# Kernel optimization log

Hardware: AMD Instinct MI355X
Metric: run time of the kernel (lower is better)

The kernel has to match this reference:

```python
import jax, jax.numpy as jnp
import numpy as np
from jax import lax

NEG = -9.0e15
ALPHA = 0.2  # LeakyReLU slope

def _cnn(x, conv1_w, conv1_b, conv2_w, conv2_b):
    # x: (BN,1,9,9)
    dn = ('NCHW', 'OIHW', 'NCHW')
    y = lax.conv_general_dilated(x, conv1_w, (1, 1), 'SAME', dimension_numbers=dn)
    y = jax.nn.relu(y + conv1_b[None, :, None, None])
    y = lax.conv_general_dilated(y, conv2_w, (1, 1), 'VALID', dimension_numbers=dn)
    y = jax.nn.relu(y + conv2_b[None, :, None, None])
    return y.reshape(y.shape[0], -1)  # (BN, 32*7*7=1568)

def _gat(h, adj, W, a1, a2):
    # h: (B,N,F) ; adj: (B,N,N) int
    Wh = h @ W                                  # (B,N,D)
    # a([Wh_i ; Wh_j]) == Wh_i@a1 + Wh_j@a2  (exact split of the concat linear)
    s1 = Wh @ a1                                # (B,N) query-node term
    s2 = Wh @ a2                                # (B,N) key-node term
    e = jax.nn.leaky_relu(s1[:, :, None] + s2[:, None, :], ALPHA)  # (B,N,N)
    e = jnp.where(adj > 0, e, NEG)
    attn = jax.nn.softmax(e, axis=-1)           # dropout off (eval mode)
    h_prime = jnp.einsum('bij,bjd->bid', attn, Wh)
    return jax.nn.elu(h_prime)

def reference(obs_grids, adj_matrix, conv1_w, conv1_b, conv2_w, conv2_b,
              W, a1, a2, actor_w, actor_b, critic_w, critic_b):
    B, N, C, H, Wd = obs_grids.shape
    feats = _cnn(obs_grids.reshape(B * N, C, H, Wd), conv1_w, conv1_b, conv2_w, conv2_b)
    feats = feats.reshape(B, N, -1)             # (B,N,1568)
    emb = _gat(feats, adj_matrix, W, a1, a2)    # (B,N,64)
    logits = emb @ actor_w + actor_b            # (B,N,n_actions)
    values = emb @ critic_w + critic_b          # (B,N,1)
    return (logits, values)

def setup_inputs() -> dict:
    key = jax.random.key(0)
    ks = jax.random.split(key, 12)
    B, N, H, Wd = 8, 1024, 9, 9
    FEAT, HID, NA = 1568, 64, 16
    f32 = jnp.float32
    inp = {}
    inp['obs_grids'] = jax.random.normal(ks[0], (B, N, 1, H, Wd), f32)
    inp['adj_matrix'] = jax.random.randint(ks[1], (B, N, N), 0, 2, jnp.int32)
    inp['conv1_w'] = jax.random.normal(ks[2], (16, 1, 3, 3), f32) * 0.1
    inp['conv1_b'] = jnp.zeros((16,), f32)
    inp['conv2_w'] = jax.random.normal(ks[3], (32, 16, 3, 3), f32) * 0.05
    inp['conv2_b'] = jnp.zeros((32,), f32)
    inp['W'] = jax.random.normal(ks[4], (FEAT, HID), f32) * (1.0 / np.sqrt(FEAT))
    inp['a1'] = jax.random.normal(ks[5], (HID,), f32) * 0.1
    inp['a2'] = jax.random.normal(ks[6], (HID,), f32) * 0.1
    inp['actor_w'] = jax.random.normal(ks[7], (HID, NA), f32) * (1.0 / np.sqrt(HID))
    inp['actor_b'] = jnp.zeros((NA,), f32)
    inp['critic_w'] = jax.random.normal(ks[8], (HID, 1), f32) * (1.0 / np.sqrt(HID))
    inp['critic_b'] = jnp.zeros((1,), f32)
    return inp
```

## Files before the change

kernel.cpp:

```cpp
#include <hip/hip_runtime.h>
#include <math.h>

#define NEG_BIG (-9.0e15f)

typedef __attribute__((ext_vector_type(8))) short short8;
typedef __attribute__((ext_vector_type(4))) short short4v;
typedef __attribute__((ext_vector_type(4))) float f32x4;

__device__ __forceinline__ short f32_to_bf16_bits(float f) {
  union { float f; unsigned u; } cv; cv.f = f;
  unsigned r = (cv.u + 0x7fffu + ((cv.u >> 16) & 1u)) >> 16;
  return (short)r;
}

__global__ __launch_bounds__(256) void wt_prep(const float* __restrict__ W,
                                               short* __restrict__ Wt) {
  int idx = blockIdx.x * 256 + threadIdx.x;
  if (idx < 1568 * 64) {
    int k = idx >> 6, n = idx & 63;
    Wt[n * 1568 + k] = f32_to_bf16_bits(W[idx]);
  }
}

#define IPB 8
#define FSTR 1608
__global__ __launch_bounds__(256) void cnn_gemm_kernel(
    const float* __restrict__ obs, const float* __restrict__ w1,
    const float* __restrict__ b1, const float* __restrict__ w2,
    const float* __restrict__ b2, const short* __restrict__ Wt,
    const float* __restrict__ a1, const float* __restrict__ a2,
    short* __restrict__ Whb, float* __restrict__ s1, float* __restrict__ s2)
{
  __shared__ float sw1[144];
  __shared__ float sb1[16];
  __shared__ float sb2[32];
  __shared__ __align__(16) short wt[32 * 160];
  __shared__ float sinp[IPB * 121];
  __shared__ __align__(16) short ubuf[IPB * FSTR];
  int tid = threadIdx.x;
  long inst0 = (long)blockIdx.x * IPB;

  for (int i = tid; i < 144; i += 256) sw1[i] = w1[i];
  if (tid < 16) sb1[tid] = b1[tid];
  if (tid < 32) sb2[tid] = b2[tid];
  for (int i = tid; i < 32 * 160; i += 256) {
    int o = i / 160, kp = i - o * 160;
    int kstep = kp >> 5, which = (kp >> 4) & 1, ci = kp & 15;
    int tap = kstep * 2 + which;
    float v = (tap < 9) ? w2[o * 144 + ci * 9 + tap] : 0.0f;
    wt[i] = f32_to_bf16_bits(v);
  }
  for (int i = tid; i < IPB * 121; i += 256) {
    int inst = i / 121, rem = i - inst * 121;
    int py = rem / 11, px = rem - py * 11;
    float v = 0.f;
    if (py >= 1 && py <= 9 && px >= 1 && px <= 9)
      v = obs[(inst0 + inst) * 81 + (py - 1) * 9 + (px - 1)];
    sinp[inst * 121 + rem] = v;
  }
  __syncthreads();

  {
    int inst = tid >> 5, s = tid & 31;
    const float* ib = &sinp[inst * 121];
    short* hw = &ubuf[inst * FSTR];
    for (int c = 0; c < 16; ++c) {
      float wk[9];
      #pragma unroll
      for (int k = 0; k < 9; ++k) wk[k] = sw1[c * 9 + k];
      float bias = sb1[c];
      #pragma unroll
      for (int t = 0; t < 3; ++t) {
        int px = s + t * 32;
        if (px < 81) {
          int y = (px * 456) >> 12;
          const float* ip = ib + px + 2 * y;
          float a = bias
            + ip[0]  * wk[0] + ip[1]  * wk[1] + ip[2]  * wk[2]
            + ip[11] * wk[3] + ip[12] * wk[4] + ip[13] * wk[5]
            + ip[22] * wk[6] + ip[23] * wk[7] + ip[24] * wk[8];
          a = fmaxf(a, 0.f);
          int idx = (px * 16 + c) ^ (((px >> 2) & 3) << 3);
          hw[idx] = f32_to_bf16_bits(a);
        }
      }
    }
  }

  int lane = tid & 63;
  int wv = tid >> 6;
  int g = lane >> 4;
  int which = g >> 1;
  int half = g & 1;
  int colr = lane & 15;

  const int offtab[9] = {0, 1, 2, 9, 10, 11, 18, 19, 20};
  int myoff[5];
  #pragma unroll
  for (int k = 0; k < 5; ++k) {
    int tap = k * 2 + which;
    myoff[k] = (tap < 9) ? offtab[tap] : 0;
  }
  int posm[4];
  #pragma unroll
  for (int mt = 0; mt < 4; ++mt) {
    int p = mt * 16 + colr;
    posm[mt] = (p < 49) ? (p / 7) * 9 + (p % 7) : 0;
  }
  short8 bfw[2][5];
  #pragma unroll
  for (int nt = 0; nt < 2; ++nt)
    #pragma unroll
    for (int k = 0; k < 5; ++k)
      bfw[nt][k] = *(const short8*)&wt[(nt * 16 + colr) * 160 + k * 32 + g * 8];

  #pragma unroll
  for (int ii = 0; ii < 2; ++ii) {
    int inst = wv * 2 + ii;
    const short* hb = &ubuf[inst * FSTR];
    short* fb = &ubuf[inst * FSTR];
    f32x4 acc[4][2];
    #pragma unroll
    for (int mt = 0; mt < 4; ++mt) {
      short8 af[5];
      #pragma unroll
      for (int k = 0; k < 5; ++k) {
        int row = posm[mt] + myoff[k];
        int idx = (row * 16 + half * 8) ^ (((row >> 2) & 3) << 3);
        af[k] = *(const short8*)&hb[idx];
      }
      #pragma unroll
      for (int nt = 0; nt < 2; ++nt) {
        f32x4 a0 = {0.f, 0.f, 0.f, 0.f};
        #pragma unroll
        for (int k = 0; k < 5; ++k)
          a0 = __builtin_amdgcn_mfma_f32_16x16x32_bf16(af[k], bfw[nt][k], a0, 0, 0, 0);
        acc[mt][nt] = a0;
      }
    }
    #pragma unroll
    for (int mt = 0; mt < 4; ++mt) {
      #pragma unroll
      for (int nt = 0; nt < 2; ++nt) {
        int o = nt * 16 + colr;
        float bias = sb2[o];
        #pragma unroll
        for (int r = 0; r < 4; ++r) {
          int p = mt * 16 + g * 4 + r;
          if (p < 49)
            fb[o * 49 + p] = f32_to_bf16_bits(fmaxf(acc[mt][nt][r] + bias, 0.f));
        }
      }
    }
  }
  __syncthreads();

  {
    int arow = colr & 7;
    const short* Wrow = Wt + (wv * 16 + colr) * 1568;
    f32x4 acc2 = {0.f, 0.f, 0.f, 0.f};
    for (int ks = 0; ks < 49; ++ks) {
      short8 af = *(const short8*)&ubuf[arow * FSTR + ks * 32 + g * 8];
      short8 bf = *(const short8*)&Wrow[ks * 32 + g * 8];
      acc2 = __builtin_amdgcn_mfma_f32_16x16x32_bf16(af, bf, acc2, 0, 0, 0);
    }
    float a1c = a1[wv * 16 + colr];
    float a2c = a2[wv * 16 + colr];
    float* sp1 = sinp;
    float* sp2 = sinp + 32;
    if (g < 2) {
      long bidx = inst0 >> 10;
      int node0 = (int)(inst0 & 1023) + g * 4;
      short4v pk;
      #pragma unroll
      for (int r = 0; r < 4; ++r) pk[r] = f32_to_bf16_bits(acc2[r]);
      *(short4v*)&Whb[(bidx * 64 + wv * 16 + colr) * 1024 + node0] = pk;
      #pragma unroll
      for (int r = 0; r < 4; ++r) {
        int inst = g * 4 + r;
        float v = acc2[r];
        float x1 = v * a1c, x2 = v * a2c;
        #pragma unroll
        for (int w = 1; w < 16; w <<= 1) { x1 += __shfl_xor(x1, w); x2 += __shfl_xor(x2, w); }
        if (colr == 0) { sp1[wv * 8 + inst] = x1; sp2[wv * 8 + inst] = x2; }
      }
    }
  }
  __syncthreads();
  if (tid < 8) {
    float* sp1 = sinp;
    float* sp2 = sinp + 32;
    s1[inst0 + tid] = sp1[tid] + sp1[8 + tid] + sp1[16 + tid] + sp1[24 + tid];
    s2[inst0 + tid] = sp2[tid] + sp2[8 + tid] + sp2[16 + tid] + sp2[24 + tid];
  }
}

#define PSTR2 1096
__global__ __launch_bounds__(256) void gat_kernel(
    const int* __restrict__ adj, const short* __restrict__ Whb,
    const float* __restrict__ s1, const float* __restrict__ s2,
    const float* __restrict__ actor_w, const float* __restrict__ actor_b,
    const float* __restrict__ critic_w, const float* __restrict__ critic_b,
    float* __restrict__ out)
{
  __shared__ __align__(16) short pb[16 * PSTR2];
  __shared__ __align__(16) float s2s[1024];
  __shared__ float saw[64 * 16];
  __shared__ float scw[64];
  __shared__ float sab[16];
  __shared__ float denom[16];
  __shared__ float emb[16][65];
  int tid = threadIdx.x;
  int b = blockIdx.y;
  int i0 = blockIdx.x * 16;

  for (int j = tid; j < 1024; j += 256) s2s[j] = s2[b * 1024 + j];
  for (int idx2 = tid; idx2 < 64 * 16; idx2 += 256) saw[idx2] = actor_w[idx2];
  if (tid < 64) scw[tid] = critic_w[tid];
  if (tid < 16) sab[tid] = actor_b[tid];
  __syncthreads();

  {
    int il = tid >> 4, r = tid & 15;
    int i = i0 + il;
    float s1i = s1[b * 1024 + i];
    const int* arow = adj + ((long)(b * 1024 + i)) * 1024;
    unsigned long long amask = 0ull;
    float m = -3.0e38f;
    #pragma unroll
    for (int jj = 0; jj < 16; ++jj) {
      int j0 = jj * 64 + r * 4;
      int4 a4 = *(const int4*)&arow[j0];
      float4 sv = *(const float4*)&s2s[j0];
      float e0 = s1i + sv.x; e0 = (e0 > 0.f) ? e0 : 0.2f * e0;
      float e1 = s1i + sv.y; e1 = (e1 > 0.f) ? e1 : 0.2f * e1;
      float e2 = s1i + sv.z; e2 = (e2 > 0.f) ? e2 : 0.2f * e2;
      float e3 = s1i + sv.w; e3 = (e3 > 0.f) ? e3 : 0.2f * e3;
      if (a4.x > 0) { m = fmaxf(m, e0); amask |= 1ull << (jj * 4 + 0); }
      if (a4.y > 0) { m = fmaxf(m, e1); amask |= 1ull << (jj * 4 + 1); }
      if (a4.z > 0) { m = fmaxf(m, e2); amask |= 1ull << (jj * 4 + 2); }
      if (a4.w > 0) { m = fmaxf(m, e3); amask |= 1ull << (jj * 4 + 3); }
    }
    #pragma unroll
    for (int w = 1; w < 16; w <<= 1) m = fmaxf(m, __shfl_xor(m, w));
    float sum = 0.f;
    short* prow = &pb[il * PSTR2];
    #pragma unroll
    for (int jj = 0; jj < 16; ++jj) {
      int j0 = jj * 64 + r * 4;
      float4 sv = *(const float4*)&s2s[j0];
      float e0 = s1i + sv.x; e0 = (e0 > 0.f) ? e0 : 0.2f * e0;
      float e1 = s1i + sv.y; e1 = (e1 > 0.f) ? e1 : 0.2f * e1;
      float e2 = s1i + sv.z; e2 = (e2 > 0.f) ? e2 : 0.2f * e2;
      float e3 = s1i + sv.w; e3 = (e3 > 0.f) ? e3 : 0.2f * e3;
      float p0 = ((amask >> (jj * 4 + 0)) & 1ull) ? __expf(e0 - m) : 0.f;
      float p1 = ((amask >> (jj * 4 + 1)) & 1ull) ? __expf(e1 - m) : 0.f;
      float p2 = ((amask >> (jj * 4 + 2)) & 1ull) ? __expf(e2 - m) : 0.f;
      float p3 = ((amask >> (jj * 4 + 3)) & 1ull) ? __expf(e3 - m) : 0.f;
      sum += (p0 + p1) + (p2 + p3);
      short4v st;
      st[0] = f32_to_bf16_bits(p0); st[1] = f32_to_bf16_bits(p1);
      st[2] = f32_to_bf16_bits(p2); st[3] = f32_to_bf16_bits(p3);
      *(short4v*)&prow[j0] = st;
    }
    #pragma unroll
    for (int w = 1; w < 16; w <<= 1) sum += __shfl_xor(sum, w);
    if (r == 0) denom[il] = sum;
  }
  __syncthreads();

  {
    int lane = tid & 63, wv = tid >> 6, g = lane >> 4, colr = lane & 15;
    const short* Wcol = Whb + ((long)b * 64 + wv * 16 + colr) * 1024;
    const short* prow = &pb[colr * PSTR2];
    f32x4 acc = {0.f, 0.f, 0.f, 0.f};
    #pragma unroll
    for (int ks = 0; ks < 32; ++ks) {
      short8 af = *(const short8*)&prow[ks * 32 + g * 8];
      short8 bf = *(const short8*)&Wcol[ks * 32 + g * 8];
      acc = __builtin_amdgcn_mfma_f32_16x16x32_bf16(af, bf, acc, 0, 0, 0);
    }
    #pragma unroll
    for (int rr = 0; rr < 4; ++rr) {
      int row = g * 4 + rr;
      float v = acc[rr] / denom[row];
      v = (v > 0.f) ? v : expm1f(v);
      emb[row][wv * 16 + colr] = v;
    }
  }
  __syncthreads();

  {
    int il = tid >> 4, na = tid & 15;
    float accl = sab[na];
    #pragma unroll
    for (int d = 0; d < 64; ++d) accl += emb[il][d] * saw[d * 16 + na];
    out[((long)(b * 1024 + i0 + il)) * 16 + na] = accl;
  }
  if (tid < 16) {
    float v = critic_b[0];
    #pragma unroll
    for (int d = 0; d < 64; ++d) v += emb[tid][d] * scw[d];
    out[131072 + b * 1024 + i0 + tid] = v;
  }
}

extern "C" void kernel_launch(void* const* d_in, const int* in_sizes, int n_in,
                              void* d_out, int out_size, void* d_ws, size_t ws_size,
                              hipStream_t stream)
{
  const float* obs = (const float*)d_in[0];
  const int*   adj = (const int*)d_in[1];
  const float* c1w = (const float*)d_in[2];
  const float* c1b = (const float*)d_in[3];
  const float* c2w = (const float*)d_in[4];
  const float* c2b = (const float*)d_in[5];
  const float* W   = (const float*)d_in[6];
  const float* a1  = (const float*)d_in[7];
  const float* a2  = (const float*)d_in[8];
  const float* aw  = (const float*)d_in[9];
  const float* ab  = (const float*)d_in[10];
  const float* cw  = (const float*)d_in[11];
  const float* cb  = (const float*)d_in[12];
  float* out = (float*)d_out;
  float* ws = (float*)d_ws;

  short* Whb = (short*)ws;
  float* s1  = ws + 262144;
  float* s2  = s1 + 8192;
  short* Wt  = (short*)(s2 + 8192);

  hipLaunchKernelGGL(wt_prep, dim3((1568 * 64 + 255) / 256), dim3(256), 0, stream, W, Wt);
  hipLaunchKernelGGL(cnn_gemm_kernel, dim3(1024), dim3(256), 0, stream,
                     obs, c1w, c1b, c2w, c2b, Wt, a1, a2, Whb, s1, s2);
  hipLaunchKernelGGL(gat_kernel, dim3(64, 8), dim3(256), 0, stream,
                     adj, Whb, s1, s2, aw, ab, cw, cb, out);
}
```

Baseline: 67.69 us.

## Pad CNN feature layout to 52 per channel and vectorize conv stores

Repacks the projection weight and the per-instance feature buffer so each of the 32 channels occupies 52 bf16 slots (49 valid plus zero padding). This allows conv2 outputs to be written as packed 4-element stores instead of guarded scalar stores. Conv1 now caches its input patch in registers, loads weights and bias as float4 vectors from a padded LDS table, and writes two channels per 32-bit store. The trade-off is that the projection GEMM runs 52 MFMA k-steps instead of 49, and the padded region must be zeroed in shared memory, which also grows LDS use.

```diff
diff --git a/kernel.cpp b/kernel.cpp
--- a/kernel.cpp
+++ b/kernel.cpp
@@ -13,17 +13,20 @@
   return (short)r;
 }
 
+#define KPAD 1664
 __global__ __launch_bounds__(256) void wt_prep(const float* __restrict__ W,
                                                short* __restrict__ Wt) {
   int idx = blockIdx.x * 256 + threadIdx.x;
-  if (idx < 1568 * 64) {
-    int k = idx >> 6, n = idx & 63;
-    Wt[n * 1568 + k] = f32_to_bf16_bits(W[idx]);
+  if (idx < 64 * KPAD) {
+    int n = idx / KPAD, kk = idx - n * KPAD;
+    int o = kk / 52, p = kk - o * 52;
+    float v = (p < 49) ? W[(o * 49 + p) * 64 + n] : 0.0f;
+    Wt[idx] = f32_to_bf16_bits(v);
   }
 }
 
 #define IPB 8
-#define FSTR 1608
+#define FSTR 1672
 __global__ __launch_bounds__(256) void cnn_gemm_kernel(
     const float* __restrict__ obs, const float* __restrict__ w1,
     const float* __restrict__ b1, const float* __restrict__ w2,
@@ -31,8 +34,7 @@
     const float* __restrict__ a1, const float* __restrict__ a2,
     short* __restrict__ Whb, float* __restrict__ s1, float* __restrict__ s2)
 {
-  __shared__ float sw1[144];
-  __shared__ float sb1[16];
+  __shared__ __align__(16) float sw1p[192];
   __shared__ float sb2[32];
   __shared__ __align__(16) short wt[32 * 160];
   __shared__ float sinp[IPB * 121];
@@ -40,8 +42,11 @@
   int tid = threadIdx.x;
   long inst0 = (long)blockIdx.x * IPB;
 
-  for (int i = tid; i < 144; i += 256) sw1[i] = w1[i];
-  if (tid < 16) sb1[tid] = b1[tid];
+  for (int i = tid; i < 192; i += 256) {
+    int c = i / 12, k = i - c * 12;
+    float v = (k < 9) ? w1[c * 9 + k] : ((k == 9) ? b1[c] : 0.0f);
+    sw1p[i] = v;
+  }
   if (tid < 32) sb2[tid] = b2[tid];
   for (int i = tid; i < 32 * 160; i += 256) {
     int o = i / 160, kp = i - o * 160;
@@ -58,30 +63,54 @@
       v = obs[(inst0 + inst) * 81 + (py - 1) * 9 + (px - 1)];
     sinp[inst * 121 + rem] = v;
   }
+  for (int i = tid; i < IPB * 188; i += 256) {
+    int inst = i / 188, q = i - inst * 188;
+    *(unsigned*)&ubuf[inst * FSTR + 1296 + q * 2] = 0u;
+  }
   __syncthreads();
 
   {
     int inst = tid >> 5, s = tid & 31;
     const float* ib = &sinp[inst * 121];
     short* hw = &ubuf[inst * FSTR];
-    for (int c = 0; c < 16; ++c) {
-      float wk[9];
-      #pragma unroll
-      for (int k = 0; k < 9; ++k) wk[k] = sw1[c * 9 + k];
-      float bias = sb1[c];
+    float inr[3][9];
+    #pragma unroll
+    for (int t = 0; t < 3; ++t) {
+      int px = s + t * 32;
+      if (px < 81) {
+        int y = (px * 456) >> 12;
+        const float* ip = ib + px + 2 * y;
+        inr[t][0] = ip[0];  inr[t][1] = ip[1];  inr[t][2] = ip[2];
+        inr[t][3] = ip[11]; inr[t][4] = ip[12]; inr[t][5] = ip[13];
+        inr[t][6] = ip[22]; inr[t][7] = ip[23]; inr[t][8] = ip[24];
+      }
+    }
+    #pragma unroll
+    for (int cp = 0; cp < 8; ++cp) {
+      int c0 = cp * 2, c1 = cp * 2 + 1;
+      float4 wa0 = *(const float4*)&sw1p[c0 * 12];
+      float4 wb0 = *(const float4*)&sw1p[c0 * 12 + 4];
+      float4 wc0 = *(const float4*)&sw1p[c0 * 12 + 8];
+      float4 wa1 = *(const float4*)&sw1p[c1 * 12];
+      float4 wb1 = *(const float4*)&sw1p[c1 * 12 + 4];
+      float4 wc1 = *(const float4*)&sw1p[c1 * 12 + 8];
       #pragma unroll
       for (int t = 0; t < 3; ++t) {
         int px = s + t * 32;
         if (px < 81) {
-          int y = (px * 456) >> 12;
-          const float* ip = ib + px + 2 * y;
-          float a = bias
-            + ip[0]  * wk[0] + ip[1]  * wk[1] + ip[2]  * wk[2]
-            + ip[11] * wk[3] + ip[12] * wk[4] + ip[13] * wk[5]
-            + ip[22] * wk[6] + ip[23] * wk[7] + ip[24] * wk[8];
-          a = fmaxf(a, 0.f);
-          int idx = (px * 16 + c) ^ (((px >> 2) & 3) << 3);
-          hw[idx] = f32_to_bf16_bits(a);
+          float v0 = wc0.y
+            + inr[t][0] * wa0.x + inr[t][1] * wa0.y + inr[t][2] * wa0.z
+            + inr[t][3] * wa0.w + inr[t][4] * wb0.x + inr[t][5] * wb0.y
+            + inr[t][6] * wb0.z + inr[t][7] * wb0.w + inr[t][8] * wc0.x;
+          float v1 = wc1.y
+            + inr[t][0] * wa1.x + inr[t][1] * wa1.y + inr[t][2] * wa1.z
+            + inr[t][3] * wa1.w + inr[t][4] * wb1.x + inr[t][5] * wb1.y
+            + inr[t][6] * wb1.z + inr[t][7] * wb1.w + inr[t][8] * wc1.x;
+          v0 = fmaxf(v0, 0.f); v1 = fmaxf(v1, 0.f);
+          unsigned pk = (unsigned)(unsigned short)f32_to_bf16_bits(v0)
+                      | ((unsigned)(unsigned short)f32_to_bf16_bits(v1) << 16);
+          int idx = (px * 16 + c0) ^ (((px >> 2) & 3) << 3);
+          *(unsigned*)&hw[idx] = pk;
         }
       }
     }
@@ -139,17 +168,23 @@
       }
     }
     #pragma unroll
-    for (int mt = 0; mt < 4; ++mt) {
+    for (int mt = 0; mt < 3; ++mt) {
       #pragma unroll
       for (int nt = 0; nt < 2; ++nt) {
         int o = nt * 16 + colr;
         float bias = sb2[o];
+        short4v pk;
         #pragma unroll
-        for (int r = 0; r < 4; ++r) {
-          int p = mt * 16 + g * 4 + r;
-          if (p < 49)
-            fb[o * 49 + p] = f32_to_bf16_bits(fmaxf(acc[mt][nt][r] + bias, 0.f));
-        }
+        for (int r = 0; r < 4; ++r)
+          pk[r] = f32_to_bf16_bits(fmaxf(acc[mt][nt][r] + bias, 0.f));
+        *(short4v*)&fb[o * 52 + mt * 16 + g * 4] = pk;
+      }
+    }
+    if (g == 0) {
+      #pragma unroll
+      for (int nt = 0; nt < 2; ++nt) {
+        int o = nt * 16 + colr;
+        fb[o * 52 + 48] = f32_to_bf16_bits(fmaxf(acc[3][nt][0] + sb2[o], 0.f));
       }
     }
   }
@@ -157,9 +192,9 @@
 
   {
     int arow = colr & 7;
-    const short* Wrow = Wt + (wv * 16 + colr) * 1568;
+    const short* Wrow = Wt + (wv * 16 + colr) * KPAD;
     f32x4 acc2 = {0.f, 0.f, 0.f, 0.f};
-    for (int ks = 0; ks < 49; ++ks) {
+    for (int ks = 0; ks < 52; ++ks) {
       short8 af = *(const short8*)&ubuf[arow * FSTR + ks * 32 + g * 8];
       short8 bf = *(const short8*)&Wrow[ks * 32 + g * 8];
       acc2 = __builtin_amdgcn_mfma_f32_16x16x32_bf16(af, bf, acc2, 0, 0, 0);
@@ -330,7 +365,7 @@
   float* s2  = s1 + 8192;
   short* Wt  = (short*)(s2 + 8192);
 
-  hipLaunchKernelGGL(wt_prep, dim3((1568 * 64 + 255) / 256), dim3(256), 0, stream, W, Wt);
+  hipLaunchKernelGGL(wt_prep, dim3((64 * KPAD + 255) / 256), dim3(256), 0, stream, W, Wt);
   hipLaunchKernelGGL(cnn_gemm_kernel, dim3(1024), dim3(256), 0, stream,
                      obs, c1w, c1b, c2w, c2b, Wt, a1, a2, Whb, s1, s2);
   hipLaunchKernelGGL(gat_kernel, dim3(64, 8), dim3(256), 0, stream,
```

Result: slower. 83.01 us (+22.6%).
